# Kernel tuning notes

Measured on AMD Instinct MI355X. Metric: run time of the kernel, lower is better.

Reference implementation:

```python
import jax, jax.numpy as jnp
import numpy as np

BAND_WIDTH = 0.5
EPS = 1e-5
NORM_EPS = 1e-12  # F.normalize eps


def setup_inputs() -> dict:
    key = jax.random.key(0)
    k1, k2 = jax.random.split(key)
    shape = (8, 512, 48, 48)  # N, C, H, W  (VGG conv4_4 features of a 384x384 image)
    return {
        "pred": jax.random.normal(k1, shape, dtype=jnp.float32),
        "target": jax.random.normal(k2, shape, dtype=jnp.float32),
    }


def reference(pred, target):
    N, C, H, W = pred.shape
    # center both by target channel-mean over (N, H, W)
    y_mu = jnp.mean(target, axis=(0, 2, 3), keepdims=True)
    x_c = pred - y_mu
    y_c = target - y_mu
    # L2-normalize along channel dim (F.normalize: divide by max(norm, eps))
    x_n = x_c / jnp.maximum(jnp.linalg.norm(x_c, axis=1, keepdims=True), NORM_EPS)
    y_n = y_c / jnp.maximum(jnp.linalg.norm(y_c, axis=1, keepdims=True), NORM_EPS)
    x_v = x_n.reshape(N, C, H * W)
    y_v = y_n.reshape(N, C, H * W)
    # pairwise cosine distance: [N, HW, HW]
    cosine_sim = jnp.einsum('ncp,ncq->npq', x_v, y_v)
    dist_raw = 1.0 - cosine_sim
    # relative distance: divide each row by its min over keys (dim=2)
    dist_min = jnp.min(dist_raw, axis=2, keepdims=True)
    dist_tilde = dist_raw / (dist_min + EPS)
    # similarity + row-normalize (softmax-like over dim=2)
    w = jnp.exp((1.0 - dist_tilde) / BAND_WIDTH)
    cx = w / jnp.sum(w, axis=2, keepdims=True)
    # max over query dim (dim=1), mean over key dim -> [N]
    cx = jnp.mean(jnp.max(cx, axis=1), axis=1)
    cx_loss = -jnp.log(cx + EPS)
    # reduction='mean', loss_weight=1.0
    return jnp.mean(cx_loss)
```

## Files before the change

### kernel.cpp

```cpp
#include <hip/hip_runtime.h>
#include <stdint.h>

#define NB 8
#define CC 512
#define PP 2304
#define EPSF 1e-5f
#define RCH 12

typedef short bf16x8 __attribute__((ext_vector_type(8)));
typedef float f32x4 __attribute__((ext_vector_type(4)));

typedef __attribute__((address_space(3))) uint8_t lds8_t;
typedef __attribute__((address_space(1))) const uint8_t g8_t;

__device__ __forceinline__ void async16(void* lds, const void* g) {
  __builtin_amdgcn_global_load_lds((g8_t*)g, (lds8_t*)lds, 16, 0, 0);
}

__device__ __forceinline__ float bf2lo(uint32_t u) { return __uint_as_float(u << 16); }
__device__ __forceinline__ float bf2hi(uint32_t u) { return __uint_as_float(u & 0xffff0000u); }
__device__ __forceinline__ uint32_t f2bf(float f) {
  uint32_t u = __float_as_uint(f);
  return (u + 0x7fffu + ((u >> 16) & 1u)) >> 16;
}

template <int N>
__device__ __forceinline__ void vmwait() {
  if constexpr (N == 0) asm volatile("s_waitcnt vmcnt(0)" ::: "memory");
  else if constexpr (N == 4) asm volatile("s_waitcnt vmcnt(4)" ::: "memory");
  else if constexpr (N == 6) asm volatile("s_waitcnt vmcnt(6)" ::: "memory");
  else if constexpr (N == 8) asm volatile("s_waitcnt vmcnt(8)" ::: "memory");
}

__global__ __launch_bounds__(256) void k_cast(
    const float* __restrict__ pred, const float* __restrict__ tgt,
    uint16_t* __restrict__ xt, uint16_t* __restrict__ yt,
    float* __restrict__ ssx, float* __restrict__ ssy, float* __restrict__ musum) {
  __shared__ uint32_t lt[64][33];
  __shared__ float red[4][64];
  const int p0 = blockIdx.x * 64, c0 = blockIdx.y * 64, n = blockIdx.z;
  const int t = threadIdx.x, lp = t & 63, cb = t >> 6;
  for (int which = 0; which < 2; ++which) {
    const float* in = which ? tgt : pred;
    uint16_t* out = which ? yt : xt;
    float* ss = which ? ssy : ssx;
    float sq = 0.f;
    uint32_t packs[8];
#pragma unroll
    for (int i = 0; i < 16; ++i) {
      const int c = c0 + cb * 16 + i;
      float v = in[((size_t)n * CC + c) * PP + p0 + lp];
      sq += v * v;
      uint32_t b = f2bf(v);
      if (i & 1) packs[i >> 1] |= b << 16; else packs[i >> 1] = b;
    }
#pragma unroll
    for (int j = 0; j < 8; ++j) lt[lp][cb * 8 + j] = packs[j];
    red[cb][lp] = sq;
    __syncthreads();
    if (t < 64)
      atomicAdd(&ss[(size_t)n * PP + p0 + t],
                red[0][t] + red[1][t] + red[2][t] + red[3][t]);
    if (which && t < 32) {
      float s0 = 0.f, s1 = 0.f;
      for (int p = 0; p < 64; ++p) {
        const uint32_t u = lt[p][t];
        s0 += bf2lo(u); s1 += bf2hi(u);
      }
      atomicAdd(&musum[c0 + 2 * t], s0);
      atomicAdd(&musum[c0 + 2 * t + 1], s1);
    }
    const int p = t >> 2, ch = t & 3;
    uint4 v0, v1;
    v0.x = lt[p][ch * 8 + 0]; v0.y = lt[p][ch * 8 + 1];
    v0.z = lt[p][ch * 8 + 2]; v0.w = lt[p][ch * 8 + 3];
    v1.x = lt[p][ch * 8 + 4]; v1.y = lt[p][ch * 8 + 5];
    v1.z = lt[p][ch * 8 + 6]; v1.w = lt[p][ch * 8 + 7];
    uint4* ob = (uint4*)(out + (((size_t)n * PP + p0 + p) * CC + c0 + ch * 16));
    ob[0] = v0; ob[1] = v1;
    __syncthreads();
  }
}

__global__ __launch_bounds__(256) void k_gemv(
    const float* __restrict__ musum,
    const uint16_t* __restrict__ xt, const uint16_t* __restrict__ yt,
    float* __restrict__ mvx, float* __restrict__ mvy) {
  const uint16_t* T = blockIdx.y ? yt : xt;
  float* mv = blockIdx.y ? mvy : mvx;
  __shared__ float mu_l[512];
  __shared__ float m2red[4];
  const int t = threadIdx.x, w = t >> 6, lane = t & 63;
  const float scale = 1.0f / (NB * PP);
  float m2p = 0.f;
  for (int i = t; i < 512; i += 256) {
    float m = musum[i] * scale;
    mu_l[i] = m;
    m2p += m * m;
  }
#pragma unroll
  for (int d = 1; d < 64; d <<= 1) m2p += __shfl_xor(m2p, d);
  if (lane == 0) m2red[w] = m2p;
  __syncthreads();
  const float mu2h = 0.5f * (m2red[0] + m2red[1] + m2red[2] + m2red[3]);
  for (int it = 0; it < 16; ++it) {
    const int r = blockIdx.x * 64 + w * 16 + it;
    uint4 u = *(const uint4*)(T + (size_t)r * CC + lane * 8);
    float s = 0.f;
    const float* m = &mu_l[lane * 8];
    s += bf2lo(u.x) * m[0] + bf2hi(u.x) * m[1];
    s += bf2lo(u.y) * m[2] + bf2hi(u.y) * m[3];
    s += bf2lo(u.z) * m[4] + bf2hi(u.z) * m[5];
    s += bf2lo(u.w) * m[6] + bf2hi(u.w) * m[7];
#pragma unroll
    for (int d = 1; d < 64; d <<= 1) s += __shfl_xor(s, d);
    if (lane == 0) mv[r] = s - mu2h;
  }
}

__device__ __forceinline__ void stage_half(uint16_t* dst, const uint16_t* g, int tid) {
  async16((char*)dst + tid * 16, g);
  async16((char*)dst + tid * 16 + 8192, g + 64 * CC);
}

template <int QM, int QN, bool LA, bool LB, bool STG, int VM>
__device__ __forceinline__ void phase(const uint16_t (*R)[8192],
                                      uint16_t* sdst, const uint16_t* ssrc,
                                      int tid, int lane, int wr, int wcn,
                                      bf16x8 (&af)[4][2], bf16x8 (&bf)[2][2][2],
                                      f32x4 (&acc)[2][4][2][2]) {
  if (LA) {
#pragma unroll
    for (int i = 0; i < 4; ++i) {
      const int rh = wr * 64 + i * 16 + (lane & 15);
      const char* base = (const char*)R[QM] + rh * 128;
      const int sw = (rh & 7) << 4;
#pragma unroll
      for (int kk = 0; kk < 2; ++kk)
        af[i][kk] = *(const bf16x8*)(base + ((kk * 64 + (lane >> 4) * 16) ^ sw));
    }
  }
  if (LB) {
#pragma unroll
    for (int j = 0; j < 2; ++j) {
      const int rh = wcn * 32 + j * 16 + (lane & 15);
      const char* base = (const char*)R[2 + QN] + rh * 128;
      const int sw = (rh & 7) << 4;
#pragma unroll
      for (int kk = 0; kk < 2; ++kk)
        bf[QN][j][kk] = *(const bf16x8*)(base + ((kk * 64 + (lane >> 4) * 16) ^ sw));
    }
  }
  if (STG) stage_half(sdst, ssrc, tid);
  __builtin_amdgcn_s_barrier();
  asm volatile("s_waitcnt lgkmcnt(0)" ::: "memory");
  __builtin_amdgcn_s_setprio(1);
#pragma unroll
  for (int i = 0; i < 4; ++i)
#pragma unroll
    for (int j = 0; j < 2; ++j)
#pragma unroll
      for (int kk = 0; kk < 2; ++kk)
        acc[QM][i][QN][j] = __builtin_amdgcn_mfma_f32_16x16x32_bf16(
            af[i][kk], bf[QN][j][kk], acc[QM][i][QN][j], 0, 0, 0);
  __builtin_amdgcn_s_setprio(0);
  vmwait<VM>();
  __builtin_amdgcn_s_barrier();
}

__global__ __launch_bounds__(512, 2) void k_gemm(
    const uint16_t* __restrict__ xt, const uint16_t* __restrict__ yt,
    const float* __restrict__ ssx, const float* __restrict__ ssy,
    const float* __restrict__ mvx, const float* __restrict__ mvy,
    uint16_t* __restrict__ S) {
  __shared__ uint16_t lds[2][4][8192];
  int flat = blockIdx.x + 9 * blockIdx.y + 81 * blockIdx.z;
  flat = (flat & 7) * 81 + (flat >> 3);
  const int nb = flat / 81;
  const int rem = flat - nb * 81;
  const int m0 = (rem % 9) * 256, n0 = (rem / 9) * 256;
  const int tid = threadIdx.x, lane = tid & 63, wid = tid >> 6;
  const int wr = wid >> 2, wcn = wid & 3;
  const uint16_t* Ax = xt + (size_t)nb * PP * CC;
  const uint16_t* By = yt + (size_t)nb * PP * CC;
  const int lswz = (tid & 7) ^ ((tid >> 3) & 7);
  const uint16_t* gAb = Ax + (size_t)(m0 + (tid >> 3)) * CC + lswz * 8;
  const uint16_t* gBb = By + (size_t)(n0 + (tid >> 3)) * CC + lswz * 8;

  f32x4 acc[2][4][2][2];
#pragma unroll
  for (int a = 0; a < 2; ++a)
#pragma unroll
    for (int b = 0; b < 4; ++b)
#pragma unroll
      for (int c = 0; c < 2; ++c)
#pragma unroll
        for (int d = 0; d < 2; ++d) acc[a][b][c][d] = (f32x4){0.f, 0.f, 0.f, 0.f};

  stage_half(lds[0][0], gAb, tid);
  stage_half(lds[0][2], gBb, tid);
  stage_half(lds[0][1], gAb + 128 * CC, tid);
  stage_half(lds[0][3], gBb + 128 * CC, tid);
  stage_half(lds[1][0], gAb + 64, tid);
  stage_half(lds[1][2], gBb + 64, tid);
  vmwait<8>();
  __builtin_amdgcn_s_barrier();

  bf16x8 af[4][2], bf[2][2][2];
  for (int kt = 0; kt < 6; ++kt) {
    const int cur = kt & 1;
    const uint16_t(*R)[8192] = lds[cur];
    uint16_t(*Wn)[8192] = lds[cur ^ 1];
    uint16_t(*Wc)[8192] = lds[cur];
    const int ko = (kt + 1) * 64;
    phase<0, 0, true, true, true, 6>(R, Wn[1], gAb + 128 * CC + ko, tid, lane, wr, wcn, af, bf, acc);
    phase<0, 1, false, true, true, -1>(R, Wn[3], gBb + 128 * CC + ko, tid, lane, wr, wcn, af, bf, acc);
    phase<1, 0, true, false, true, -1>(R, Wc[0], gAb + ko + 64, tid, lane, wr, wcn, af, bf, acc);
    phase<1, 1, false, false, true, 8>(R, Wc[2], gBb + ko + 64, tid, lane, wr, wcn, af, bf, acc);
  }
  {
    const uint16_t(*R)[8192] = lds[0];
    phase<0, 0, true, true, true, 6>(R, lds[1][1], gAb + 128 * CC + 7 * 64, tid, lane, wr, wcn, af, bf, acc);
    phase<0, 1, false, true, true, -1>(R, lds[1][3], gBb + 128 * CC + 7 * 64, tid, lane, wr, wcn, af, bf, acc);
    phase<1, 0, true, false, false, -1>(R, nullptr, nullptr, tid, lane, wr, wcn, af, bf, acc);
    phase<1, 1, false, false, false, 4>(R, nullptr, nullptr, tid, lane, wr, wcn, af, bf, acc);
  }
  {
    const uint16_t(*R)[8192] = lds[1];
    phase<0, 0, true, true, false, 0>(R, nullptr, nullptr, tid, lane, wr, wcn, af, bf, acc);
    phase<0, 1, false, true, false, -1>(R, nullptr, nullptr, tid, lane, wr, wcn, af, bf, acc);
    phase<1, 0, true, false, false, -1>(R, nullptr, nullptr, tid, lane, wr, wcn, af, bf, acc);
    phase<1, 1, false, false, false, -1>(R, nullptr, nullptr, tid, lane, wr, wcn, af, bf, acc);
  }

  const float* rsp = ssx + (size_t)nb * PP + m0;
  const float* csp = ssy + (size_t)nb * PP + n0;
  const float* mvr = mvx + (size_t)nb * PP + m0;
  const float* mvc = mvy + (size_t)nb * PP + n0;
  uint16_t* Sp = S + (size_t)nb * PP * PP;
  float cinv[2][2], cmv[2][2];
#pragma unroll
  for (int qn = 0; qn < 2; ++qn)
#pragma unroll
    for (int j = 0; j < 2; ++j) {
      const int col = qn * 128 + wcn * 32 + j * 16 + (lane & 15);
      const float m = mvc[col];
      cmv[qn][j] = m;
      cinv[qn][j] = 1.0f / fmaxf(sqrtf(csp[col] - 2.0f * m), 1e-12f);
    }
#pragma unroll
  for (int qm = 0; qm < 2; ++qm)
#pragma unroll
    for (int i = 0; i < 4; ++i)
#pragma unroll
      for (int r = 0; r < 4; ++r) {
        const int row = qm * 128 + wr * 64 + i * 16 + (lane >> 4) * 4 + r;
        const float mr = mvr[row];
        const float rinv = 1.0f / fmaxf(sqrtf(rsp[row] - 2.0f * mr), 1e-12f);
        uint16_t* orow = Sp + (size_t)(m0 + row) * PP + n0;
#pragma unroll
        for (int qn = 0; qn < 2; ++qn)
#pragma unroll
          for (int j = 0; j < 2; ++j)
            orow[qn * 128 + wcn * 32 + j * 16 + (lane & 15)] = (uint16_t)f2bf(
                (acc[qm][i][qn][j][r] - mr - cmv[qn][j]) * rinv * cinv[qn][j]);
      }
}

__global__ __launch_bounds__(256) void k_rowcol(const uint16_t* __restrict__ S,
                                                int* __restrict__ cxcol) {
  const int pc = blockIdx.x, n = blockIdx.y;
  __shared__ uint16_t wlds[RCH][PP];
  __shared__ float lri[RCH];
  const int t = threadIdx.x, w = t >> 6, lane = t & 63;
  const size_t Sn = (size_t)n * PP * PP + (size_t)pc * 24 * PP;
  float best0[5], best1[5];
#pragma unroll
  for (int i = 0; i < 5; ++i) { best0[i] = 0.f; best1[i] = 0.f; }
  for (int half = 0; half < 2; ++half) {
    for (int it = 0; it < 3; ++it) {
      const int r = w * 3 + it;
      const uint2* rp = (const uint2*)(S + Sn + (size_t)(half * RCH + r) * PP);
      uint2 u[9];
#pragma unroll
      for (int k = 0; k < 9; ++k) u[k] = rp[lane + k * 64];
      float v[36];
#pragma unroll
      for (int k = 0; k < 9; ++k) {
        v[4 * k + 0] = bf2lo(u[k].x); v[4 * k + 1] = bf2hi(u[k].x);
        v[4 * k + 2] = bf2lo(u[k].y); v[4 * k + 3] = bf2hi(u[k].y);
      }
      float mx = v[0];
#pragma unroll
      for (int k = 1; k < 36; ++k) mx = fmaxf(mx, v[k]);
#pragma unroll
      for (int d = 1; d < 64; d <<= 1) mx = fmaxf(mx, __shfl_xor(mx, d));
      const float sc = 2.0f / (1.0f - mx + EPSF);
      const float b = (EPSF - mx) * sc;
      float s = 0.f;
#pragma unroll
      for (int k = 0; k < 9; ++k) {
        const float w0 = __expf(fmaf(v[4 * k + 0], sc, b));
        const float w1 = __expf(fmaf(v[4 * k + 1], sc, b));
        const float w2 = __expf(fmaf(v[4 * k + 2], sc, b));
        const float w3 = __expf(fmaf(v[4 * k + 3], sc, b));
        s += (w0 + w1) + (w2 + w3);
        uint2 wp;
        wp.x = f2bf(w0) | (f2bf(w1) << 16);
        wp.y = f2bf(w2) | (f2bf(w3) << 16);
        ((uint2*)&wlds[r][0])[lane + k * 64] = wp;
      }
#pragma unroll
      for (int d = 1; d < 64; d <<= 1) s += __shfl_xor(s, d);
      if (lane == 0) lri[r] = 1.0f / s;
    }
    __syncthreads();
#pragma unroll
    for (int i = 0; i < 5; ++i) {
      const int pi = t + i * 256;
      if (pi < PP / 2) {
        float b0 = best0[i], b1 = best1[i];
#pragma unroll
        for (int r = 0; r < RCH; ++r) {
          const uint32_t u = ((const uint32_t*)&wlds[r][0])[pi];
          const float ri = lri[r];
          b0 = fmaxf(b0, bf2lo(u) * ri);
          b1 = fmaxf(b1, bf2hi(u) * ri);
        }
        best0[i] = b0; best1[i] = b1;
      }
    }
    __syncthreads();
  }
#pragma unroll
  for (int i = 0; i < 5; ++i) {
    const int pi = t + i * 256;
    if (pi < PP / 2) {
      atomicMax(&cxcol[n * PP + 2 * pi], __float_as_int(best0[i]));
      atomicMax(&cxcol[n * PP + 2 * pi + 1], __float_as_int(best1[i]));
    }
  }
}

__global__ __launch_bounds__(512) void k_fin(const int* __restrict__ cxcol,
                                             float* __restrict__ out) {
  __shared__ float red[8];
  const int t = threadIdx.x, w = t >> 6, lane = t & 63;
  float s = 0.f;
  for (int q = lane; q < PP; q += 64) s += __int_as_float(cxcol[w * PP + q]);
#pragma unroll
  for (int d = 1; d < 64; d <<= 1) s += __shfl_xor(s, d);
  if (lane == 0) red[w] = -logf(s * (1.0f / PP) + EPSF);
  __syncthreads();
  if (t == 0) {
    float a = 0.f;
#pragma unroll
    for (int n = 0; n < NB; ++n) a += red[n];
    out[0] = a * (1.0f / NB);
  }
}

extern "C" void kernel_launch(void* const* d_in, const int* in_sizes, int n_in,
                              void* d_out, int out_size, void* d_ws, size_t ws_size,
                              hipStream_t stream) {
  const float* pred = (const float*)d_in[0];
  const float* tgt  = (const float*)d_in[1];
  float* W = (float*)d_ws;
  float* musum = W + 0;
  float* ssx   = W + 512;
  float* ssy   = W + 18944;
  int*   cxcol = (int*)(W + 37376);
  float* mvx   = W + 56320;
  float* mvy   = W + 74752;
  uint16_t* xt = (uint16_t*)(W + 93440);
  uint16_t* yt = xt + (size_t)NB * PP * CC;
  uint16_t* S  = yt + (size_t)NB * PP * CC;

  hipMemsetAsync(W, 0, 55808 * sizeof(float), stream);

  k_cast<<<dim3(PP / 64, CC / 64, NB), dim3(256), 0, stream>>>(
      pred, tgt, xt, yt, ssx, ssy, musum);
  k_gemv<<<dim3(288, 2), dim3(256), 0, stream>>>(musum, xt, yt, mvx, mvy);
  k_gemm<<<dim3(9, 9, NB), dim3(512), 0, stream>>>(xt, yt, ssx, ssy, mvx, mvy, S);
  k_rowcol<<<dim3(96, NB), dim3(256), 0, stream>>>(S, cxcol);
  k_fin<<<dim3(1), dim3(512), 0, stream>>>(cxcol, (float*)d_out);
}
```

Before: 157.7 us.

## Single-buffer GEMM LDS tiles with in-place staging to raise occupancy

Replaces the double-buffered 128KB LDS layout in the similarity GEMM with a single 64KB buffer. Each quarter tile is refilled in place as soon as the phase that reads it has finished, and the vmcnt waits are retuned to match. The launch bound moves from 2 to 4 blocks per CU, aiming to fit more blocks per CU so other blocks hide memory latency. The cost is a shallower prefetch: loads for the next k-step have less time to land before they are needed, and register pressure tightens under the higher occupancy bound.

```diff
diff --git a/kernel.cpp b/kernel.cpp
--- a/kernel.cpp
+++ b/kernel.cpp
@@ -27,9 +27,9 @@
 template <int N>
 __device__ __forceinline__ void vmwait() {
   if constexpr (N == 0) asm volatile("s_waitcnt vmcnt(0)" ::: "memory");
+  else if constexpr (N == 2) asm volatile("s_waitcnt vmcnt(2)" ::: "memory");
   else if constexpr (N == 4) asm volatile("s_waitcnt vmcnt(4)" ::: "memory");
   else if constexpr (N == 6) asm volatile("s_waitcnt vmcnt(6)" ::: "memory");
-  else if constexpr (N == 8) asm volatile("s_waitcnt vmcnt(8)" ::: "memory");
 }
 
 __global__ __launch_bounds__(256) void k_cast(
@@ -123,9 +123,10 @@
   async16((char*)dst + tid * 16 + 8192, g + 64 * CC);
 }
 
-template <int QM, int QN, bool LA, bool LB, bool STG, int VM>
+template <int QM, int QN, bool LA, bool LB, int VM>
 __device__ __forceinline__ void phase(const uint16_t (*R)[8192],
-                                      uint16_t* sdst, const uint16_t* ssrc,
+                                      uint16_t* d1, const uint16_t* s1,
+                                      uint16_t* d2, const uint16_t* s2,
                                       int tid, int lane, int wr, int wcn,
                                       bf16x8 (&af)[4][2], bf16x8 (&bf)[2][2][2],
                                       f32x4 (&acc)[2][4][2][2]) {
@@ -151,7 +152,8 @@
         bf[QN][j][kk] = *(const bf16x8*)(base + ((kk * 64 + (lane >> 4) * 16) ^ sw));
     }
   }
-  if (STG) stage_half(sdst, ssrc, tid);
+  if (d1) stage_half(d1, s1, tid);
+  if (d2) stage_half(d2, s2, tid);
   __builtin_amdgcn_s_barrier();
   asm volatile("s_waitcnt lgkmcnt(0)" ::: "memory");
   __builtin_amdgcn_s_setprio(1);
@@ -168,12 +170,12 @@
   __builtin_amdgcn_s_barrier();
 }
 
-__global__ __launch_bounds__(512, 2) void k_gemm(
+__global__ __launch_bounds__(512, 4) void k_gemm(
     const uint16_t* __restrict__ xt, const uint16_t* __restrict__ yt,
     const float* __restrict__ ssx, const float* __restrict__ ssy,
     const float* __restrict__ mvx, const float* __restrict__ mvy,
     uint16_t* __restrict__ S) {
-  __shared__ uint16_t lds[2][4][8192];
+  __shared__ uint16_t lds[4][8192];
   int flat = blockIdx.x + 9 * blockIdx.y + 81 * blockIdx.z;
   flat = (flat & 7) * 81 + (flat >> 3);
   const int nb = flat / 81;
@@ -197,40 +199,35 @@
 #pragma unroll
         for (int d = 0; d < 2; ++d) acc[a][b][c][d] = (f32x4){0.f, 0.f, 0.f, 0.f};
 
-  stage_half(lds[0][0], gAb, tid);
-  stage_half(lds[0][2], gBb, tid);
-  stage_half(lds[0][1], gAb + 128 * CC, tid);
-  stage_half(lds[0][3], gBb + 128 * CC, tid);
-  stage_half(lds[1][0], gAb + 64, tid);
-  stage_half(lds[1][2], gBb + 64, tid);
-  vmwait<8>();
+  stage_half(lds[0], gAb, tid);
+  stage_half(lds[2], gBb, tid);
+  stage_half(lds[3], gBb + 128 * CC, tid);
+  stage_half(lds[1], gAb + 128 * CC, tid);
+  vmwait<4>();
   __builtin_amdgcn_s_barrier();
 
   bf16x8 af[4][2], bf[2][2][2];
-  for (int kt = 0; kt < 6; ++kt) {
-    const int cur = kt & 1;
-    const uint16_t(*R)[8192] = lds[cur];
-    uint16_t(*Wn)[8192] = lds[cur ^ 1];
-    uint16_t(*Wc)[8192] = lds[cur];
+  const uint16_t(*R)[8192] = lds;
+  for (int kt = 0; kt < 7; ++kt) {
     const int ko = (kt + 1) * 64;
-    phase<0, 0, true, true, true, 6>(R, Wn[1], gAb + 128 * CC + ko, tid, lane, wr, wcn, af, bf, acc);
-    phase<0, 1, false, true, true, -1>(R, Wn[3], gBb + 128 * CC + ko, tid, lane, wr, wcn, af, bf, acc);
-    phase<1, 0, true, false, true, -1>(R, Wc[0], gAb + ko + 64, tid, lane, wr, wcn, af, bf, acc);
-    phase<1, 1, false, false, true, 8>(R, Wc[2], gBb + ko + 64, tid, lane, wr, wcn, af, bf, acc);
+    phase<0, 0, true, true, 2>(R, nullptr, nullptr, nullptr, nullptr,
+                               tid, lane, wr, wcn, af, bf, acc);
+    phase<0, 1, false, true, 2>(R, lds[0], gAb + ko, nullptr, nullptr,
+                                tid, lane, wr, wcn, af, bf, acc);
+    phase<1, 0, true, false, -1>(R, lds[2], gBb + ko, lds[3], gBb + 128 * CC + ko,
+                                 tid, lane, wr, wcn, af, bf, acc);
+    phase<1, 1, false, false, 4>(R, lds[1], gAb + 128 * CC + ko, nullptr, nullptr,
+                                 tid, lane, wr, wcn, af, bf, acc);
   }
   {
-    const uint16_t(*R)[8192] = lds[0];
-    phase<0, 0, true, true, true, 6>(R, lds[1][1], gAb + 128 * CC + 7 * 64, tid, lane, wr, wcn, af, bf, acc);
-    phase<0, 1, false, true, true, -1>(R, lds[1][3], gBb + 128 * CC + 7 * 64, tid, lane, wr, wcn, af, bf, acc);
-    phase<1, 0, true, false, false, -1>(R, nullptr, nullptr, tid, lane, wr, wcn, af, bf, acc);
-    phase<1, 1, false, false, false, 4>(R, nullptr, nullptr, tid, lane, wr, wcn, af, bf, acc);
-  }
-  {
-    const uint16_t(*R)[8192] = lds[1];
-    phase<0, 0, true, true, false, 0>(R, nullptr, nullptr, tid, lane, wr, wcn, af, bf, acc);
-    phase<0, 1, false, true, false, -1>(R, nullptr, nullptr, tid, lane, wr, wcn, af, bf, acc);
-    phase<1, 0, true, false, false, -1>(R, nullptr, nullptr, tid, lane, wr, wcn, af, bf, acc);
-    phase<1, 1, false, false, false, -1>(R, nullptr, nullptr, tid, lane, wr, wcn, af, bf, acc);
+    phase<0, 0, true, true, 2>(R, nullptr, nullptr, nullptr, nullptr,
+                               tid, lane, wr, wcn, af, bf, acc);
+    phase<0, 1, false, true, 0>(R, nullptr, nullptr, nullptr, nullptr,
+                                tid, lane, wr, wcn, af, bf, acc);
+    phase<1, 0, true, false, -1>(R, nullptr, nullptr, nullptr, nullptr,
+                                 tid, lane, wr, wcn, af, bf, acc);
+    phase<1, 1, false, false, -1>(R, nullptr, nullptr, nullptr, nullptr,
+                                  tid, lane, wr, wcn, af, bf, acc);
   }
 
   const float* rsp = ssx + (size_t)nb * PP + m0;
```

Result: slower. 424.7 us (+169.4%).
